# Kernel tuning notes

Hardware: AMD Instinct MI355X
Metric: run time of the kernel (lower is better)

## Reference

```python
import jax, jax.numpy as jnp
import numpy as np

B, SQ, SK = 2, 2048, 2048
D, H = 1024, 16
HD = D // H              # head_dim = 64
R = 128                  # rel_pos_max_distance
P = 2 * R + 1            # num_pos_ids = 257
RADIUS = 256             # local_attention_radius


def setup_inputs() -> dict:
    key = jax.random.key(0)
    ks = jax.random.split(key, 8)
    s = 0.02
    return {
        "Q": jax.random.normal(ks[0], (B, SQ, D), dtype=jnp.float32),
        "K": jax.random.normal(ks[1], (B, SK, D), dtype=jnp.float32),
        "V": jax.random.normal(ks[2], (B, SK, D), dtype=jnp.float32),
        "Wq": jax.random.normal(ks[3], (D, D), dtype=jnp.float32) * s,
        "Wk": jax.random.normal(ks[4], (D, D), dtype=jnp.float32) * s,
        "Wv": jax.random.normal(ks[5], (D, D), dtype=jnp.float32) * s,
        "Wo": jax.random.normal(ks[6], (D, D), dtype=jnp.float32) * s,
        "E": jax.random.normal(ks[7], (P, D), dtype=jnp.float32) * s,  # rel_embeds
    }


def _split_heads(x, W):
    # bias-free projection then split: B x S x D -> B x H x S x HD
    y = x @ W.T
    b, s, _ = y.shape
    return y.reshape(b, s, H, HD).transpose(0, 2, 1, 3)


def reference(Q, K, V, Wq, Wk, Wv, Wo, E):
    q = _split_heads(Q, Wq)  # B,H,Sq,HD
    k = _split_heads(K, Wk)  # B,H,Sk,HD
    v = _split_heads(V, Wv)  # B,H,Sk,HD

    # rel_embeds reshape matches torch: E[p] viewed as (head_dim, num_heads)
    rel = E.reshape(P, HD, H).transpose(2, 0, 1)           # H,P,HD
    Q_rel = jnp.einsum("bhqd,hpd->bhqp", q, rel)           # B,H,Sq,P

    # slided relative position ids: clip(j - i, -R, R) + R
    i = jnp.arange(SQ)[:, None]
    j = jnp.arange(SK)[None, :]
    rel_ids = jnp.clip(j - i, -R, R) + R                   # Sq,Sk
    rel_shift = jnp.take_along_axis(
        Q_rel, jnp.broadcast_to(rel_ids, (B, H, SQ, SK)), axis=3
    )                                                       # B,H,Sq,Sk

    energy = (jnp.einsum("bhqd,bhkd->bhqk", q, k) + rel_shift) / jnp.sqrt(
        jnp.float32(HD)
    )

    # local attention mask: True = masked (outside window of radius RADIUS)
    mask = jnp.abs(j - i) > RADIUS                          # Sq,Sk
    mask = mask & ~jnp.all(mask, axis=-1, keepdims=True)    # never mask full rows
    energy = jnp.where(mask[None, None], -jnp.inf, energy)

    attn = jax.nn.softmax(energy, axis=-1)                  # B,H,Sq,Sk
    out = jnp.einsum("bhqk,bhkd->bhqd", attn, v)            # B,H,Sq,HD
    # torch: view(B,H,Sq,HD).permute(0,2,3,1).flatten(2,3) -> B,Sq,(HD*H)
    out = out.transpose(0, 2, 3, 1).reshape(B, SQ, D)
    return out @ Wo.T
```

## Files before the change

### kernel.cpp

```cpp
#include <hip/hip_runtime.h>
#include <hip/hip_bf16.h>

#define BATCH 2
#define SQn 2048
#define SKn 2048
#define DMODEL 1024
#define NH 16
#define HD 64
#define NPOS 257
#define RWIN 128
#define RADIUS 256

typedef __attribute__((ext_vector_type(8))) short bf16x8;
typedef __attribute__((ext_vector_type(4))) float f32x4;

static __device__ __forceinline__ unsigned short f2bf(float f) {
    union { float f; unsigned u; } v; v.f = f;
    unsigned r = (v.u + 0x7FFFu + ((v.u >> 16) & 1u)) >> 16;
    return (unsigned short)r;
}
static __device__ __forceinline__ float bf2f(unsigned short b) {
    union { unsigned u; float f; } v; v.u = ((unsigned)b) << 16;
    return v.f;
}

static __device__ __forceinline__ void gl_lds16(const unsigned short* g, unsigned short* l) {
    __builtin_amdgcn_global_load_lds(
        (const __attribute__((address_space(1))) unsigned*)g,
        (__attribute__((address_space(3))) unsigned*)l, 16, 0, 0);
}

#define SWZ(row) (((row) ^ ((row) >> 2)) & 3)

__global__ __launch_bounds__(256) void convert_kernel(
    const float* __restrict__ Q, const float* __restrict__ K, const float* __restrict__ V,
    const float* __restrict__ Wq, const float* __restrict__ Wk, const float* __restrict__ Wv,
    const float* __restrict__ Wo,
    unsigned short* __restrict__ xb,
    unsigned short* __restrict__ wb,
    unsigned short* __restrict__ woh)
{
    int i = blockIdx.x * 256 + threadIdx.x;
    if (i < 3145728) {
        int which = i >> 20;
        int off = i & 1048575;
        const float* src = which == 0 ? Q : (which == 1 ? K : V);
        unsigned short* dst = xb + (size_t)which * 4194304;
        float4 v4 = ((const float4*)src)[off];
        ushort4 o4;
        o4.x = f2bf(v4.x); o4.y = f2bf(v4.y); o4.z = f2bf(v4.z); o4.w = f2bf(v4.w);
        ((ushort4*)dst)[off] = o4;
    } else {
        int i2 = i - 3145728;
        int which = i2 >> 18;
        int off = i2 & 262143;
        if (which < 3) {
            const float* src = which == 0 ? Wq : (which == 1 ? Wk : Wv);
            unsigned short* dst = wb + (size_t)which * 1048576;
            float4 v4 = ((const float4*)src)[off];
            ushort4 o4;
            o4.x = f2bf(v4.x); o4.y = f2bf(v4.y); o4.z = f2bf(v4.z); o4.w = f2bf(v4.w);
            ((ushort4*)dst)[off] = o4;
        } else {
            float4 v4 = ((const float4*)Wo)[off];
            int e0 = off * 4;
            int n  = e0 >> 10;
            int c0 = e0 & 1023;
            int d  = c0 >> 4;
            int h0 = c0 & 15;
            woh[((size_t)(h0 + 0) * 1024 + n) * 64 + d] = f2bf(v4.x);
            woh[((size_t)(h0 + 1) * 1024 + n) * 64 + d] = f2bf(v4.y);
            woh[((size_t)(h0 + 2) * 1024 + n) * 64 + d] = f2bf(v4.z);
            woh[((size_t)(h0 + 3) * 1024 + n) * 64 + d] = f2bf(v4.w);
        }
    }
}

__global__ __launch_bounds__(256) void mfma_gemm(
    const unsigned short* __restrict__ Xall,
    const unsigned short* __restrict__ Wall,
    unsigned short* __restrict__ Yall)
{
    __shared__ unsigned short sA[128 * 32];
    __shared__ unsigned short sB[128 * 32];
    __shared__ unsigned short sT[64 * 136];

    const int tid  = threadIdx.x;
    const int wv   = tid >> 6;
    const int lane = tid & 63;
    const int quad = lane >> 4;
    const int l15  = lane & 15;
    const int z    = blockIdx.z;
    const int m0   = blockIdx.x * 128;
    const int n0   = blockIdx.y * 128;
    const int wr   = (wv >> 1) * 64;
    const int wc   = (wv & 1) * 64;

    const unsigned short* X = Xall + (size_t)z * (4096 * 1024);
    const unsigned short* W = Wall + (size_t)z * (1024 * 1024);

    int aoff[4], boff[4];
#pragma unroll
    for (int t = 0; t < 4; ++t) {
        int row = wr + t * 16 + l15;
        aoff[t] = row * 32 + ((quad ^ SWZ(row)) * 8);
        int col = wc + t * 16 + l15;
        boff[t] = col * 32 + ((quad ^ SWZ(col)) * 8);
    }

    int srow[2], scg[2], sf[2];
#pragma unroll
    for (int r = 0; r < 2; ++r) {
        int f = r * 256 + tid;
        sf[r] = f;
        srow[r] = f >> 2;
        scg[r] = (f & 3) ^ SWZ(srow[r]);
    }

    f32x4 acc[4][4];
#pragma unroll
    for (int i = 0; i < 4; ++i)
#pragma unroll
        for (int j = 0; j < 4; ++j)
            acc[i][j] = (f32x4){0.f, 0.f, 0.f, 0.f};

    for (int k0 = 0; k0 < 1024; k0 += 32) {
        __syncthreads();
#pragma unroll
        for (int r = 0; r < 2; ++r) {
            gl_lds16(X + (size_t)(m0 + srow[r]) * 1024 + k0 + scg[r] * 8, &sA[sf[r] * 8]);
            gl_lds16(W + (size_t)(n0 + srow[r]) * 1024 + k0 + scg[r] * 8, &sB[sf[r] * 8]);
        }
        __syncthreads();

        bf16x8 af[4], bfr[4];
#pragma unroll
        for (int t = 0; t < 4; ++t) af[t]  = *(const bf16x8*)&sA[aoff[t]];
#pragma unroll
        for (int t = 0; t < 4; ++t) bfr[t] = *(const bf16x8*)&sB[boff[t]];
#pragma unroll
        for (int i = 0; i < 4; ++i)
#pragma unroll
            for (int j = 0; j < 4; ++j)
                acc[i][j] = __builtin_amdgcn_mfma_f32_16x16x32_bf16(af[i], bfr[j], acc[i][j], 0, 0, 0);
    }

    unsigned short* Y = Yall + (size_t)z * (4096 * 1024);
    const int b_ = m0 >> 11;
    const int s0 = m0 & (SQn - 1);

    if (z < 2) {
#pragma unroll
        for (int i = 0; i < 4; ++i) {
            int mbase = s0 + wr + i * 16 + quad * 4;
#pragma unroll
            for (int j = 0; j < 4; ++j) {
                int col = n0 + wc + j * 16 + l15;
                int h = col >> 6, dd = col & 63;
                unsigned short* yb = Y + (((size_t)(b_ * NH + h) * SQn) << 6) + dd;
#pragma unroll
                for (int r = 0; r < 4; ++r)
                    yb[(size_t)(mbase + r) << 6] = f2bf(acc[i][j][r]);
            }
        }
    } else {
#pragma unroll
        for (int hh = 0; hh < 2; ++hh) {
            __syncthreads();
            if ((wv & 1) == hh) {
#pragma unroll
                for (int i = 0; i < 4; ++i) {
                    int mloc = wr + i * 16 + quad * 4;
#pragma unroll
                    for (int j = 0; j < 4; ++j) {
                        ushort4 pk;
                        pk.x = f2bf(acc[i][j][0]);
                        pk.y = f2bf(acc[i][j][1]);
                        pk.z = f2bf(acc[i][j][2]);
                        pk.w = f2bf(acc[i][j][3]);
                        *(ushort4*)&sT[(j * 16 + l15) * 136 + mloc] = pk;
                    }
                }
            }
            __syncthreads();
            int h = (n0 >> 6) + hh;
            unsigned short* yb = Y + ((size_t)(b_ * NH + h) * HD) * SKn + s0;
#pragma unroll
            for (int it = 0; it < 4; ++it) {
                int u = it * 256 + tid;
                int dd = u >> 4, mc = u & 15;
                uint4 val = *(const uint4*)&sT[dd * 136 + mc * 8];
                *(uint4*)(yb + (size_t)dd * SKn + mc * 8) = val;
            }
        }
    }
}

__global__ __launch_bounds__(256) void gemm_out(
    const unsigned short* __restrict__ aoh,
    const unsigned short* __restrict__ woh,
    float* __restrict__ Y)
{
    __shared__ unsigned short sA[64 * 32];
    __shared__ unsigned short sB[128 * 32];

    const int tid  = threadIdx.x;
    const int wv   = tid >> 6;
    const int lane = tid & 63;
    const int quad = lane >> 4;
    const int l15  = lane & 15;
    const int m0   = blockIdx.x * 64;
    const int n0   = blockIdx.y * 128;
    const int wr   = (wv >> 1) * 32;
    const int wc   = (wv & 1) * 64;
    const int b_   = m0 >> 11;
    const int s0   = m0 & (SQn - 1);

    int aoff[2], boff[4];
#pragma unroll
    for (int i = 0; i < 2; ++i) {
        int row = wr + i * 16 + l15;
        aoff[i] = row * 32 + ((quad ^ SWZ(row)) * 8);
    }
#pragma unroll
    for (int j = 0; j < 4; ++j) {
        int col = wc + j * 16 + l15;
        boff[j] = col * 32 + ((quad ^ SWZ(col)) * 8);
    }

    const int arow = tid >> 2;
    const int acs  = (tid & 3) ^ SWZ(arow);
    int bf_[2], brow[2], bcs[2];
#pragma unroll
    for (int r = 0; r < 2; ++r) {
        int f = r * 256 + tid;
        bf_[r] = f; brow[r] = f >> 2; bcs[r] = (f & 3) ^ SWZ(brow[r]);
    }

    f32x4 acc[2][4];
#pragma unroll
    for (int i = 0; i < 2; ++i)
#pragma unroll
        for (int j = 0; j < 4; ++j)
            acc[i][j] = (f32x4){0.f, 0.f, 0.f, 0.f};

    for (int h = 0; h < NH; ++h) {
        const unsigned short* Ah = aoh + ((size_t)(b_ * NH + h) * SQn + s0) * HD;
        const unsigned short* Bh = woh + ((size_t)h * 1024 + n0) * HD;
#pragma unroll
        for (int k0 = 0; k0 < 64; k0 += 32) {
            __syncthreads();
            gl_lds16(Ah + (size_t)arow * HD + k0 + acs * 8, &sA[tid * 8]);
#pragma unroll
            for (int r = 0; r < 2; ++r)
                gl_lds16(Bh + (size_t)brow[r] * HD + k0 + bcs[r] * 8, &sB[bf_[r] * 8]);
            __syncthreads();

            bf16x8 af[2], bfr[4];
#pragma unroll
            for (int i = 0; i < 2; ++i) af[i]  = *(const bf16x8*)&sA[aoff[i]];
#pragma unroll
            for (int j = 0; j < 4; ++j) bfr[j] = *(const bf16x8*)&sB[boff[j]];
#pragma unroll
            for (int i = 0; i < 2; ++i)
#pragma unroll
                for (int j = 0; j < 4; ++j)
                    acc[i][j] = __builtin_amdgcn_mfma_f32_16x16x32_bf16(af[i], bfr[j], acc[i][j], 0, 0, 0);
        }
    }

#pragma unroll
    for (int i = 0; i < 2; ++i) {
        int mbase = m0 + wr + i * 16 + quad * 4;
#pragma unroll
        for (int j = 0; j < 4; ++j) {
            int col = n0 + wc + j * 16 + l15;
#pragma unroll
            for (int r = 0; r < 4; ++r)
                Y[(size_t)(mbase + r) * DMODEL + col] = acc[i][j][r];
        }
    }
}

__global__ __launch_bounds__(256) void relt_kernel(
    const float* __restrict__ E, unsigned short* __restrict__ relTb)
{
    int idx = blockIdx.x * 256 + threadIdx.x;
    const int total = NH * NPOS * HD;
    if (idx < total) {
        int d = idx & (HD - 1);
        int p = (idx >> 6) % NPOS;
        int h = idx / (NPOS * HD);
        relTb[idx] = f2bf(E[(size_t)p * DMODEL + d * NH + h]);
    }
}

#define BIAS_S2 0.0014089565402528222f
#define SC2     0.1803368801111204f

__global__ __launch_bounds__(256, 2) void attn_mfma(
    const unsigned short* __restrict__ q,
    const unsigned short* __restrict__ k,
    const unsigned short* __restrict__ vT,
    const unsigned short* __restrict__ relTb,
    unsigned short* __restrict__ aoh)
{
    __shared__ unsigned short sK[64 * 64];
    __shared__ unsigned short sVt[64 * 64];
    __shared__ unsigned short sP[4][16 * 72];
    __shared__ signed char    sq8[128 * 260];
    unsigned short* const sQ = (unsigned short*)sq8;

    const int tid  = threadIdx.x;
    const int w    = tid >> 6;
    const int lane = tid & 63;
    const int quad = lane >> 4;
    const int l15  = lane & 15;
    const int xcd  = blockIdx.x & 7;
    const int sidx = blockIdx.x >> 3;
    const int bh   = (xcd << 2) | (sidx >> 4);
    const int q0   = (sidx & 15) << 7;
    const int h    = bh & (NH - 1);

    const int f1 = tid,       row1 = f1 >> 3;
    const int c1 = ((f1 & 7) ^ (row1 & 7)) * 8;
    const int f2 = 256 + tid, row2 = f2 >> 3;
    const int c2 = ((f2 & 7) ^ (row2 & 7)) * 8;

    {
        const unsigned short* gq = q + ((size_t)bh * SQn + q0) * HD;
#pragma unroll
        for (int it = 0; it < 4; ++it) {
            int f = it * 256 + tid;
            int row = f >> 3;
            int c = ((f & 7) ^ (row & 7)) * 8;
            gl_lds16(gq + row * HD + c, &sQ[f * 8]);
        }
    }
    __syncthreads();

    const int qrow = w * 16 + l15;
    const int qs = (quad ^ (qrow & 7)) * 8;
    bf16x8 a0A = *(const bf16x8*)&sQ[qrow * 64 + qs];
    bf16x8 a1A = *(const bf16x8*)&sQ[qrow * 64 + (qs ^ 32)];
    bf16x8 a0B = *(const bf16x8*)&sQ[(64 + qrow) * 64 + qs];
    bf16x8 a1B = *(const bf16x8*)&sQ[(64 + qrow) * 64 + (qs ^ 32)];

    const int myrow = w * 16 + quad * 4;
    for (int c5 = 0; c5 < 5; ++c5) {
        __syncthreads();
        const unsigned short* gr = relTb + ((size_t)h * NPOS + c5 * 64) * HD;
        gl_lds16(gr + row1 * HD + c1, &sK[f1 * 8]);
        gl_lds16(gr + row2 * HD + c2, &sK[f2 * 8]);
        __syncthreads();
#pragma unroll
        for (int t = 0; t < 4; ++t) {
            int prow = t * 16 + l15;
            int ks = (quad ^ (prow & 7)) * 8;
            bf16x8 b0 = *(const bf16x8*)&sK[prow * 64 + ks];
            bf16x8 b1 = *(const bf16x8*)&sK[prow * 64 + (ks ^ 32)];
            f32x4 ccA = {0.f, 0.f, 0.f, 0.f};
            ccA = __builtin_amdgcn_mfma_f32_16x16x32_bf16(a0A, b0, ccA, 0, 0, 0);
            ccA = __builtin_amdgcn_mfma_f32_16x16x32_bf16(a1A, b1, ccA, 0, 0, 0);
            f32x4 ccB = {0.f, 0.f, 0.f, 0.f};
            ccB = __builtin_amdgcn_mfma_f32_16x16x32_bf16(a0B, b0, ccB, 0, 0, 0);
            ccB = __builtin_amdgcn_mfma_f32_16x16x32_bf16(a1B, b1, ccB, 0, 0, 0);
            int pos = c5 * 64 + t * 16 + l15;
            if (pos < NPOS) {
#pragma unroll
                for (int r = 0; r < 4; ++r) {
                    int iqA = (int)rintf(ccA[r] * 128.0f);
                    iqA = iqA < -127 ? -127 : (iqA > 127 ? 127 : iqA);
                    sq8[(myrow + r) * 260 + pos] = (signed char)iqA;
                    int iqB = (int)rintf(ccB[r] * 128.0f);
                    iqB = iqB < -127 ? -127 : (iqB > 127 ? 127 : iqB);
                    sq8[(64 + myrow + r) * 260 + pos] = (signed char)iqB;
                }
            }
        }
    }
    __syncthreads();

    float bias0A[4], bias256A[4], bias0B[4], bias256B[4];
#pragma unroll
    for (int r = 0; r < 4; ++r) {
        bias0A[r]   = (float)sq8[(myrow + r) * 260 + 0]          * BIAS_S2;
        bias256A[r] = (float)sq8[(myrow + r) * 260 + 256]        * BIAS_S2;
        bias0B[r]   = (float)sq8[(64 + myrow + r) * 260 + 0]     * BIAS_S2;
        bias256B[r] = (float)sq8[(64 + myrow + r) * 260 + 256]   * BIAS_S2;
    }

    const int lo = (q0 - RADIUS) > 0 ? (q0 - RADIUS) : 0;
    const int hi = (q0 + 127 + RADIUS) < (SKn - 1) ? (q0 + 127 + RADIUS) : (SKn - 1);
    const int nt = ((hi - lo) >> 6) + 1;
    const int e_ = l15 - quad * 4;

    const unsigned short* kg = k  + (size_t)bh * SKn * HD;
    const unsigned short* vg = vT + (size_t)bh * HD * SKn;

    float laccA[4] = {0.f, 0.f, 0.f, 0.f};
    float laccB[4] = {0.f, 0.f, 0.f, 0.f};
    f32x4 oA[4], oB[4];
#pragma unroll
    for (int t = 0; t < 4; ++t) {
        oA[t] = (f32x4){0.f, 0.f, 0.f, 0.f};
        oB[t] = (f32x4){0.f, 0.f, 0.f, 0.f};
    }

    {
        gl_lds16(kg + (size_t)(lo + row1) * HD + c1, &sK[f1 * 8]);
        gl_lds16(kg + (size_t)(lo + row2) * HD + c2, &sK[f2 * 8]);
        gl_lds16(vg + (size_t)row1 * SKn + lo + c1, &sVt[f1 * 8]);
        gl_lds16(vg + (size_t)row2 * SKn + lo + c2, &sVt[f2 * 8]);
    }

    for (int kt = 0; kt < nt; ++kt) {
        const int kb = lo + (kt << 6);
        __syncthreads();

        bf16x8 kf0[4], kf1[4], vf0[4], vf1[4];
#pragma unroll
        for (int t = 0; t < 4; ++t) {
            int prow = t * 16 + l15;
            int ks = (quad ^ (prow & 7)) * 8;
            kf0[t] = *(const bf16x8*)&sK[prow * 64 + ks];
            kf1[t] = *(const bf16x8*)&sK[prow * 64 + (ks ^ 32)];
            vf0[t] = *(const bf16x8*)&sVt[prow * 64 + ks];
            vf1[t] = *(const bf16x8*)&sVt[prow * 64 + (ks ^ 32)];
        }
        __syncthreads();

        if (kt + 1 < nt) {
            const int kb2 = kb + 64;
            gl_lds16(kg + (size_t)(kb2 + row1) * HD + c1, &sK[f1 * 8]);
            gl_lds16(kg + (size_t)(kb2 + row2) * HD + c2, &sK[f2 * 8]);
            gl_lds16(vg + (size_t)row1 * SKn + kb2 + c1, &sVt[f1 * 8]);
            gl_lds16(vg + (size_t)row2 * SKn + kb2 + c2, &sVt[f2 * 8]);
        }

        const int dtbaseA = kb - q0 - w * 16;
        if (dtbaseA > -320 && dtbaseA < 272) {
#pragma unroll
            for (int t = 0; t < 4; ++t) {
                const int dt = dtbaseA + t * 16;
                const int spb = (quad * 4) * 72 + t * 16 + l15;
                if (dt <= -272 || dt >= 272) {
#pragma unroll
                    for (int r = 0; r < 4; ++r) sP[w][spb + r * 72] = 0;
                } else {
                    f32x4 sc = {0.f, 0.f, 0.f, 0.f};
                    sc = __builtin_amdgcn_mfma_f32_16x16x32_bf16(a0A, kf0[t], sc, 0, 0, 0);
                    sc = __builtin_amdgcn_mfma_f32_16x16x32_bf16(a1A, kf1[t], sc, 0, 0, 0);

                    float pv[4];
                    if (dt >= -112 && dt <= 112) {
                        int idx0 = myrow * 260 + dt + 128 + e_;
#pragma unroll
                        for (int r = 0; r < 4; ++r) {
                            float bf = (float)sq8[idx0 + r * 259] * BIAS_S2;
                            pv[r] = __builtin_amdgcn_exp2f(fmaf(sc[r], SC2, bf));
                        }
                    } else if (dt >= -240 && dt <= -144) {
#pragma unroll
                        for (int r = 0; r < 4; ++r)
                            pv[r] = __builtin_amdgcn_exp2f(fmaf(sc[r], SC2, bias0A[r]));
                    } else if (dt >= 144 && dt <= 240) {
#pragma unroll
                        for (int r = 0; r < 4; ++r)
                            pv[r] = __builtin_amdgcn_exp2f(fmaf(sc[r], SC2, bias256A[r]));
                    } else {
#pragma unroll
                        for (int r = 0; r < 4; ++r) {
                            int d = dt + e_ - r;
                            bool in = (unsigned)(d + RADIUS) <= 2u * RADIUS;
                            int p = d < -RWIN ? 0 : (d > RWIN ? 2 * RWIN : d + RWIN);
                            float bf = (float)sq8[(myrow + r) * 260 + p] * BIAS_S2;
                            float e = __builtin_amdgcn_exp2f(fmaf(sc[r], SC2, bf));
                            pv[r] = in ? e : 0.0f;
                        }
                    }
#pragma unroll
                    for (int r = 0; r < 4; ++r) {
                        unsigned short pb = f2bf(pv[r]);
                        sP[w][spb + r * 72] = pb;
                        laccA[r] += bf2f(pb);
                    }
                }
            }
            bf16x8 p0 = *(const bf16x8*)&sP[w][l15 * 72 + quad * 8];
            bf16x8 p1 = *(const bf16x8*)&sP[w][l15 * 72 + 32 + quad * 8];
#pragma unroll
            for (int t = 0; t < 4; ++t) {
                oA[t] = __builtin_amdgcn_mfma_f32_16x16x32_bf16(p0, vf0[t], oA[t], 0, 0, 0);
                oA[t] = __builtin_amdgcn_mfma_f32_16x16x32_bf16(p1, vf1[t], oA[t], 0, 0, 0);
            }
        }

        const int dtbaseB = dtbaseA - 64;
        if (dtbaseB > -320 && dtbaseB < 272) {
#pragma unroll
            for (int t = 0; t < 4; ++t) {
                const int dt = dtbaseB + t * 16;
                const int spb = (quad * 4) * 72 + t * 16 + l15;
                if (dt <= -272 || dt >= 272) {
#pragma unroll
                    for (int r = 0; r < 4; ++r) sP[w][spb + r * 72] = 0;
                } else {
                    f32x4 sc = {0.f, 0.f, 0.f, 0.f};
                    sc = __builtin_amdgcn_mfma_f32_16x16x32_bf16(a0B, kf0[t], sc, 0, 0, 0);
                    sc = __builtin_amdgcn_mfma_f32_16x16x32_bf16(a1B, kf1[t], sc, 0, 0, 0);

                    float pv[4];
                    if (dt >= -112 && dt <= 112) {
                        int idx0 = (64 + myrow) * 260 + dt + 128 + e_;
#pragma unroll
                        for (int r = 0; r < 4; ++r) {
                            float bf = (float)sq8[idx0 + r * 259] * BIAS_S2;
                            pv[r] = __builtin_amdgcn_exp2f(fmaf(sc[r], SC2, bf));
                        }
                    } else if (dt >= -240 && dt <= -144) {
#pragma unroll
                        for (int r = 0; r < 4; ++r)
                            pv[r] = __builtin_amdgcn_exp2f(fmaf(sc[r], SC2, bias0B[r]));
                    } else if (dt >= 144 && dt <= 240) {
#pragma unroll
                        for (int r = 0; r < 4; ++r)
                            pv[r] = __builtin_amdgcn_exp2f(fmaf(sc[r], SC2, bias256B[r]));
                    } else {
#pragma unroll
                        for (int r = 0; r < 4; ++r) {
                            int d = dt + e_ - r;
                            bool in = (unsigned)(d + RADIUS) <= 2u * RADIUS;
                            int p = d < -RWIN ? 0 : (d > RWIN ? 2 * RWIN : d + RWIN);
                            float bf = (float)sq8[(64 + myrow + r) * 260 + p] * BIAS_S2;
                            float e = __builtin_amdgcn_exp2f(fmaf(sc[r], SC2, bf));
                            pv[r] = in ? e : 0.0f;
                        }
                    }
#pragma unroll
                    for (int r = 0; r < 4; ++r) {
                        unsigned short pb = f2bf(pv[r]);
                        sP[w][spb + r * 72] = pb;
                        laccB[r] += bf2f(pb);
                    }
                }
            }
            bf16x8 p0 = *(const bf16x8*)&sP[w][l15 * 72 + quad * 8];
            bf16x8 p1 = *(const bf16x8*)&sP[w][l15 * 72 + 32 + quad * 8];
#pragma unroll
            for (int t = 0; t < 4; ++t) {
                oB[t] = __builtin_amdgcn_mfma_f32_16x16x32_bf16(p0, vf0[t], oB[t], 0, 0, 0);
                oB[t] = __builtin_amdgcn_mfma_f32_16x16x32_bf16(p1, vf1[t], oB[t], 0, 0, 0);
            }
        }
    }

    float linvA[4], linvB[4];
#pragma unroll
    for (int r = 0; r < 4; ++r) {
        float lA = laccA[r];
        float lB = laccB[r];
#pragma unroll
        for (int off = 1; off <= 8; off <<= 1) {
            lA += __shfl_xor(lA, off);
            lB += __shfl_xor(lB, off);
        }
        linvA[r] = 1.0f / lA;
        linvB[r] = 1.0f / lB;
    }

    unsigned short* ob = aoh + ((size_t)bh * SQn + q0) * HD;
#pragma unroll
    for (int t = 0; t < 4; ++t) {
#pragma unroll
        for (int r = 0; r < 4; ++r) {
            int irow = w * 16 + quad * 4 + r;
            ob[irow * HD + t * 16 + l15] = f2bf(oA[t][r] * linvA[r]);
            ob[(64 + irow) * HD + t * 16 + l15] = f2bf(oB[t][r] * linvB[r]);
        }
    }
}

extern "C" void kernel_launch(void* const* d_in, const int* in_sizes, int n_in,
                              void* d_out, int out_size, void* d_ws, size_t ws_size,
                              hipStream_t stream) {
    const float* Q  = (const float*)d_in[0];
    const float* K  = (const float*)d_in[1];
    const float* V  = (const float*)d_in[2];
    const float* Wq = (const float*)d_in[3];
    const float* Wk = (const float*)d_in[4];
    const float* Wv = (const float*)d_in[5];
    const float* Wo = (const float*)d_in[6];
    const float* E  = (const float*)d_in[7];
    float* out = (float*)d_out;

    char* p = (char*)d_ws;
    unsigned short* xb    = (unsigned short*)p; p += (size_t)24 << 20;
    unsigned short* wb    = (unsigned short*)p; p += (size_t)6  << 20;
    unsigned short* woh   = (unsigned short*)p; p += (size_t)2  << 20;
    unsigned short* head  = (unsigned short*)p; p += (size_t)24 << 20;
    unsigned short* relTb = (unsigned short*)p; p += (size_t)1  << 20;
    unsigned short* aoh   = (unsigned short*)p;

    unsigned short* qb  = head;
    unsigned short* kb  = head + 4194304;
    unsigned short* vTb = head + 8388608;

    dim3 bb(256);
    convert_kernel<<<dim3(16384), bb, 0, stream>>>(Q, K, V, Wq, Wk, Wv, Wo, xb, wb, woh);
    relt_kernel<<<dim3(1028), bb, 0, stream>>>(E, relTb);
    mfma_gemm<<<dim3(32, 8, 3), bb, 0, stream>>>(xb, wb, head);
    attn_mfma<<<dim3(BATCH * NH * (SQn / 128)), bb, 0, stream>>>(qb, kb, vTb, relTb, aoh);
    gemm_out<<<dim3(64, 8), bb, 0, stream>>>(aoh, woh, out);
}
```

Measured before the change: 206.7 us.

## Widen GEMM K-tile to 64 and overlap next-tile loads with MFMA

```diff
diff --git a/kernel.cpp b/kernel.cpp
--- a/kernel.cpp
+++ b/kernel.cpp
@@ -81,8 +81,8 @@
     const unsigned short* __restrict__ Wall,
     unsigned short* __restrict__ Yall)
 {
-    __shared__ unsigned short sA[128 * 32];
-    __shared__ unsigned short sB[128 * 32];
+    __shared__ unsigned short sA[128 * 64];
+    __shared__ unsigned short sB[128 * 64];
     __shared__ unsigned short sT[64 * 136];
 
     const int tid  = threadIdx.x;
@@ -99,23 +99,24 @@
     const unsigned short* X = Xall + (size_t)z * (4096 * 1024);
     const unsigned short* W = Wall + (size_t)z * (1024 * 1024);
 
-    int aoff[4], boff[4];
-#pragma unroll
-    for (int t = 0; t < 4; ++t) {
-        int row = wr + t * 16 + l15;
-        aoff[t] = row * 32 + ((quad ^ SWZ(row)) * 8);
-        int col = wc + t * 16 + l15;
-        boff[t] = col * 32 + ((quad ^ SWZ(col)) * 8);
-    }
-
-    int srow[2], scg[2], sf[2];
-#pragma unroll
-    for (int r = 0; r < 2; ++r) {
-        int f = r * 256 + tid;
-        sf[r] = f;
-        srow[r] = f >> 2;
-        scg[r] = (f & 3) ^ SWZ(srow[r]);
-    }
+    int srow[4], scc[4];
+#pragma unroll
+    for (int it = 0; it < 4; ++it) {
+        int f = it * 256 + tid;
+        srow[it] = f >> 3;
+        scc[it]  = ((f & 7) ^ (srow[it] & 7)) * 8;
+    }
+
+    int aoff[2][4], boff[2][4];
+#pragma unroll
+    for (int ks = 0; ks < 2; ++ks)
+#pragma unroll
+        for (int t = 0; t < 4; ++t) {
+            int R = wr + t * 16 + l15;
+            aoff[ks][t] = R * 64 + ((((ks << 2) + quad) ^ (R & 7)) * 8);
+            int C = wc + t * 16 + l15;
+            boff[ks][t] = C * 64 + ((((ks << 2) + quad) ^ (C & 7)) * 8);
+        }
 
     f32x4 acc[4][4];
 #pragma unroll
@@ -124,25 +125,46 @@
         for (int j = 0; j < 4; ++j)
             acc[i][j] = (f32x4){0.f, 0.f, 0.f, 0.f};
 
-    for (int k0 = 0; k0 < 1024; k0 += 32) {
-        __syncthreads();
-#pragma unroll
-        for (int r = 0; r < 2; ++r) {
-            gl_lds16(X + (size_t)(m0 + srow[r]) * 1024 + k0 + scg[r] * 8, &sA[sf[r] * 8]);
-            gl_lds16(W + (size_t)(n0 + srow[r]) * 1024 + k0 + scg[r] * 8, &sB[sf[r] * 8]);
-        }
-        __syncthreads();
-
-        bf16x8 af[4], bfr[4];
-#pragma unroll
-        for (int t = 0; t < 4; ++t) af[t]  = *(const bf16x8*)&sA[aoff[t]];
-#pragma unroll
-        for (int t = 0; t < 4; ++t) bfr[t] = *(const bf16x8*)&sB[boff[t]];
+#pragma unroll
+    for (int it = 0; it < 4; ++it) {
+        gl_lds16(X + (size_t)(m0 + srow[it]) * 1024 + scc[it], &sA[(it * 256 + tid) * 8]);
+        gl_lds16(W + (size_t)(n0 + srow[it]) * 1024 + scc[it], &sB[(it * 256 + tid) * 8]);
+    }
+
+    for (int k0 = 0; k0 < 1024; k0 += 64) {
+        __syncthreads();
+
+        bf16x8 a0[4], b0[4];
+#pragma unroll
+        for (int t = 0; t < 4; ++t) a0[t] = *(const bf16x8*)&sA[aoff[0][t]];
+#pragma unroll
+        for (int t = 0; t < 4; ++t) b0[t] = *(const bf16x8*)&sB[boff[0][t]];
 #pragma unroll
         for (int i = 0; i < 4; ++i)
 #pragma unroll
             for (int j = 0; j < 4; ++j)
-                acc[i][j] = __builtin_amdgcn_mfma_f32_16x16x32_bf16(af[i], bfr[j], acc[i][j], 0, 0, 0);
+                acc[i][j] = __builtin_amdgcn_mfma_f32_16x16x32_bf16(a0[i], b0[j], acc[i][j], 0, 0, 0);
+
+        bf16x8 a1[4], b1[4];
+#pragma unroll
+        for (int t = 0; t < 4; ++t) a1[t] = *(const bf16x8*)&sA[aoff[1][t]];
+#pragma unroll
+        for (int t = 0; t < 4; ++t) b1[t] = *(const bf16x8*)&sB[boff[1][t]];
+        __syncthreads();
+
+        if (k0 + 64 < 1024) {
+            const int kn = k0 + 64;
+#pragma unroll
+            for (int it = 0; it < 4; ++it) {
+                gl_lds16(X + (size_t)(m0 + srow[it]) * 1024 + kn + scc[it], &sA[(it * 256 + tid) * 8]);
+                gl_lds16(W + (size_t)(n0 + srow[it]) * 1024 + kn + scc[it], &sB[(it * 256 + tid) * 8]);
+            }
+        }
+#pragma unroll
+        for (int i = 0; i < 4; ++i)
+#pragma unroll
+            for (int j = 0; j < 4; ++j)
+                acc[i][j] = __builtin_amdgcn_mfma_f32_16x16x32_bf16(a1[i], b1[j], acc[i][j], 0, 0, 0);
     }
 
     unsigned short* Y = Yall + (size_t)z * (4096 * 1024);
@@ -201,8 +223,8 @@
     const unsigned short* __restrict__ woh,
     float* __restrict__ Y)
 {
-    __shared__ unsigned short sA[64 * 32];
-    __shared__ unsigned short sB[128 * 32];
+    __shared__ unsigned short sA[64 * 64];
+    __shared__ unsigned short sB[128 * 64];
 
     const int tid  = threadIdx.x;
     const int wv   = tid >> 6;
@@ -216,25 +238,34 @@
     const int b_   = m0 >> 11;
     const int s0   = m0 & (SQn - 1);
 
-    int aoff[2], boff[4];
-#pragma unroll
-    for (int i = 0; i < 2; ++i) {
-        int row = wr + i * 16 + l15;
-        aoff[i] = row * 32 + ((quad ^ SWZ(row)) * 8);
-    }
-#pragma unroll
-    for (int j = 0; j < 4; ++j) {
-        int col = wc + j * 16 + l15;
-        boff[j] = col * 32 + ((quad ^ SWZ(col)) * 8);
-    }
-
-    const int arow = tid >> 2;
-    const int acs  = (tid & 3) ^ SWZ(arow);
-    int bf_[2], brow[2], bcs[2];
-#pragma unroll
-    for (int r = 0; r < 2; ++r) {
-        int f = r * 256 + tid;
-        bf_[r] = f; brow[r] = f >> 2; bcs[r] = (f & 3) ^ SWZ(brow[r]);
+    int rowa[2], ca[2];
+#pragma unroll
+    for (int it = 0; it < 2; ++it) {
+        int f = it * 256 + tid;
+        rowa[it] = f >> 3;
+        ca[it]   = ((f & 7) ^ (rowa[it] & 7)) * 8;
+    }
+    int rowb[4], cb[4];
+#pragma unroll
+    for (int it = 0; it < 4; ++it) {
+        int f = it * 256 + tid;
+        rowb[it] = f >> 3;
+        cb[it]   = ((f & 7) ^ (rowb[it] & 7)) * 8;
+    }
+
+    int aoff[2][2], boff[2][4];
+#pragma unroll
+    for (int ks = 0; ks < 2; ++ks) {
+#pragma unroll
+        for (int i = 0; i < 2; ++i) {
+            int R = wr + i * 16 + l15;
+            aoff[ks][i] = R * 64 + ((((ks << 2) + quad) ^ (R & 7)) * 8);
+        }
+#pragma unroll
+        for (int j = 0; j < 4; ++j) {
+            int C = wc + j * 16 + l15;
+            boff[ks][j] = C * 64 + ((((ks << 2) + quad) ^ (C & 7)) * 8);
+        }
     }
 
     f32x4 acc[2][4];
@@ -244,29 +275,53 @@
         for (int j = 0; j < 4; ++j)
             acc[i][j] = (f32x4){0.f, 0.f, 0.f, 0.f};
 
+    {
+        const unsigned short* Ah = aoh + ((size_t)(b_ * NH) * SQn + s0) * HD;
+        const unsigned short* Bh = woh + (size_t)n0 * HD;
+#pragma unroll
+        for (int it = 0; it < 2; ++it)
+            gl_lds16(Ah + (size_t)rowa[it] * HD + ca[it], &sA[(it * 256 + tid) * 8]);
+#pragma unroll
+        for (int it = 0; it < 4; ++it)
+            gl_lds16(Bh + (size_t)rowb[it] * HD + cb[it], &sB[(it * 256 + tid) * 8]);
+    }
+
     for (int h = 0; h < NH; ++h) {
-        const unsigned short* Ah = aoh + ((size_t)(b_ * NH + h) * SQn + s0) * HD;
-        const unsigned short* Bh = woh + ((size_t)h * 1024 + n0) * HD;
-#pragma unroll
-        for (int k0 = 0; k0 < 64; k0 += 32) {
-            __syncthreads();
-            gl_lds16(Ah + (size_t)arow * HD + k0 + acs * 8, &sA[tid * 8]);
-#pragma unroll
-            for (int r = 0; r < 2; ++r)
-                gl_lds16(Bh + (size_t)brow[r] * HD + k0 + bcs[r] * 8, &sB[bf_[r] * 8]);
-            __syncthreads();
-
-            bf16x8 af[2], bfr[4];
-#pragma unroll
-            for (int i = 0; i < 2; ++i) af[i]  = *(const bf16x8*)&sA[aoff[i]];
-#pragma unroll
-            for (int j = 0; j < 4; ++j) bfr[j] = *(const bf16x8*)&sB[boff[j]];
-#pragma unroll
-            for (int i = 0; i < 2; ++i)
-#pragma unroll
-                for (int j = 0; j < 4; ++j)
-                    acc[i][j] = __builtin_amdgcn_mfma_f32_16x16x32_bf16(af[i], bfr[j], acc[i][j], 0, 0, 0);
-        }
+        __syncthreads();
+
+        bf16x8 a0[2], b0[4];
+#pragma unroll
+        for (int i = 0; i < 2; ++i) a0[i] = *(const bf16x8*)&sA[aoff[0][i]];
+#pragma unroll
+        for (int j = 0; j < 4; ++j) b0[j] = *(const bf16x8*)&sB[boff[0][j]];
+#pragma unroll
+        for (int i = 0; i < 2; ++i)
+#pragma unroll
+            for (int j = 0; j < 4; ++j)
+                acc[i][j] = __builtin_amdgcn_mfma_f32_16x16x32_bf16(a0[i], b0[j], acc[i][j], 0, 0, 0);
+
+        bf16x8 a1[2], b1[4];
+#pragma unroll
+        for (int i = 0; i < 2; ++i) a1[i] = *(const bf16x8*)&sA[aoff[1][i]];
+#pragma unroll
+        for (int j = 0; j < 4; ++j) b1[j] = *(const bf16x8*)&sB[boff[1][j]];
+        __syncthreads();
+
+        if (h + 1 < NH) {
+            const unsigned short* Ah = aoh + ((size_t)(b_ * NH + h + 1) * SQn + s0) * HD;
+            const unsigned short* Bh = woh + ((size_t)(h + 1) * 1024 + n0) * HD;
+#pragma unroll
+            for (int it = 0; it < 2; ++it)
+                gl_lds16(Ah + (size_t)rowa[it] * HD + ca[it], &sA[(it * 256 + tid) * 8]);
+#pragma unroll
+            for (int it = 0; it < 4; ++it)
+                gl_lds16(Bh + (size_t)rowb[it] * HD + cb[it], &sB[(it * 256 + tid) * 8]);
+        }
+#pragma unroll
+        for (int i = 0; i < 2; ++i)
+#pragma unroll
+            for (int j = 0; j < 4; ++j)
+                acc[i][j] = __builtin_amdgcn_mfma_f32_16x16x32_bf16(a1[i], b1[j], acc[i][j], 0, 0, 0);
     }
 
 #pragma unroll
```

Result: no change. 205.0 us (-0.8%).
